# Kernel optimization log

Measured on AMD Instinct MI355X. Metric: run time of the kernel, lower is better.

## Reference

```python
import jax, jax.numpy as jnp
import numpy as np


def setup_inputs() -> dict:
    key = jax.random.key(0)
    b, d, s = 16, 1024, 4096
    x = jax.random.normal(key, (b, d, s), dtype=jnp.float32)
    return {"x": x, "k": 8}


def reference(x, k):
    # k-max pooling over the last axis, preserving original relative order.
    # torch: topk -> argsort(ind) -> gather. Equivalent: take top-k values,
    # then reorder them by ascending original index.
    vals, idx = jax.lax.top_k(x, k)            # [b, d, k]
    order = jnp.argsort(idx, axis=-1)          # positions that sort original indices ascending
    out = jnp.take_along_axis(vals, order, axis=-1)  # [b, d, k] in original order
    return out
```

## Files before the change

### kernel.cpp

```cpp
#include <hip/hip_runtime.h>
#include <stdint.h>

#define WPB    4
#define CAP    256
#define KK     8
#define SLEN   4096
#define CHUNKS 16

__global__ __launch_bounds__(256, 3)
void kmax_kernel(const float* __restrict__ x, float* __restrict__ out, int nrows) {
    const int wave = threadIdx.x >> 6;
    const int lane = threadIdx.x & 63;
    const int row  = blockIdx.x * WPB + wave;
    const bool active = row < nrows;

    __shared__ int s_cnt[WPB];
    __shared__ unsigned long long s_key[WPB][CAP];

    if (lane == 0) s_cnt[wave] = 0;
    __syncthreads();

    const float NEG_INF = __int_as_float(0xff800000);
    float Tthr = 0.0f;

    if (active) {
        const float4* xr = reinterpret_cast<const float4*>(x + (size_t)row * SLEN);
        float4 f[CHUNKS];
        #pragma unroll
        for (int j = 0; j < CHUNKS; ++j)
            f[j] = xr[j * 64 + lane];

        float m[8];
        #pragma unroll
        for (int e = 0; e < 8; ++e) m[e] = NEG_INF;
        #pragma unroll
        for (int j = 0; j < CHUNKS; ++j) {
            const int b = (j & 1) * 4;
            m[b + 0] = fmaxf(m[b + 0], f[j].x);
            m[b + 1] = fmaxf(m[b + 1], f[j].y);
            m[b + 2] = fmaxf(m[b + 2], f[j].z);
            m[b + 3] = fmaxf(m[b + 3], f[j].w);
        }

        #define MCAS(a, b) { float hi = fmaxf(m[a], m[b]); float lo = fminf(m[a], m[b]); m[a] = hi; m[b] = lo; }
        MCAS(0,1) MCAS(2,3) MCAS(4,5) MCAS(6,7)
        MCAS(0,2) MCAS(1,3) MCAS(4,6) MCAS(5,7)
        MCAS(1,2) MCAS(5,6)
        MCAS(0,4) MCAS(1,5) MCAS(2,6) MCAS(3,7)
        MCAS(2,4) MCAS(3,5)
        MCAS(1,2) MCAS(3,4) MCAS(5,6)
        #undef MCAS

        #pragma unroll
        for (int s = 1; s < 64; s <<= 1) {
            float b[8], t[8];
            #pragma unroll
            for (int i = 0; i < 8; ++i) b[i] = __shfl_xor(m[i], s, 64);
            #pragma unroll
            for (int i = 0; i < 8; ++i) t[i] = fmaxf(m[i], b[7 - i]);
            #define BCAS(a, c) { float hi = fmaxf(t[a], t[c]); float lo = fminf(t[a], t[c]); t[a] = hi; t[c] = lo; }
            BCAS(0,4) BCAS(1,5) BCAS(2,6) BCAS(3,7)
            BCAS(0,2) BCAS(1,3) BCAS(4,6) BCAS(5,7)
            BCAS(0,1) BCAS(2,3) BCAS(4,5) BCAS(6,7)
            #undef BCAS
            #pragma unroll
            for (int i = 0; i < 8; ++i) m[i] = t[i];
        }
        Tthr = m[7];

        #pragma unroll
        for (int j = 0; j < CHUNKS; ++j) {
            const float4 v = f[j];
            const bool p0 = v.x >= Tthr, p1 = v.y >= Tthr, p2 = v.z >= Tthr, p3 = v.w >= Tthr;
            if (p0 || p1 || p2 || p3) {
                const int base = (j * 64 + lane) * 4;
                #define PUSH(val, idx) { \
                    int p = atomicAdd(&s_cnt[wave], 1); \
                    if (p < CAP) { \
                        unsigned u = __float_as_uint(val); \
                        u ^= ((unsigned)((int)u >> 31)) | 0x80000000u; \
                        s_key[wave][p] = ((unsigned long long)u << 32) | (unsigned)(4095 - (idx)); \
                    } }
                if (p0) PUSH(v.x, base + 0)
                if (p1) PUSH(v.y, base + 1)
                if (p2) PUSH(v.z, base + 2)
                if (p3) PUSH(v.w, base + 3)
                #undef PUSH
            }
        }
    }

    __syncthreads();

    if (active) {
        int n = s_cnt[wave];
        if (n > CAP) n = CAP;

        unsigned long long kk[KK];
        #pragma unroll
        for (int i = 0; i < KK; ++i) kk[i] = 0ull;
        for (int i = 0; i < n; ++i) {
            unsigned long long c = s_key[wave][i];
            if (c > kk[7]) {
                #pragma unroll
                for (int t = 7; t > 0; --t)
                    kk[t] = (c > kk[t - 1]) ? kk[t - 1] : ((c > kk[t]) ? c : kk[t]);
                kk[0] = (c > kk[0]) ? c : kk[0];
            }
        }

        #define ICAS(a, b) { bool sw = (unsigned)kk[a] < (unsigned)kk[b]; \
            unsigned long long hi = sw ? kk[b] : kk[a]; \
            unsigned long long lo = sw ? kk[a] : kk[b]; \
            kk[a] = hi; kk[b] = lo; }
        ICAS(0,1) ICAS(2,3) ICAS(4,5) ICAS(6,7)
        ICAS(0,2) ICAS(1,3) ICAS(4,6) ICAS(5,7)
        ICAS(1,2) ICAS(5,6)
        ICAS(0,4) ICAS(1,5) ICAS(2,6) ICAS(3,7)
        ICAS(2,4) ICAS(3,5)
        ICAS(1,2) ICAS(3,4) ICAS(5,6)
        #undef ICAS

        if (lane == 0) {
            float vals[KK];
            #pragma unroll
            for (int i = 0; i < KK; ++i) {
                unsigned g = (unsigned)(kk[i] >> 32);
                unsigned msk = ((int)g < 0) ? 0x80000000u : 0xFFFFFFFFu;
                vals[i] = __uint_as_float(g ^ msk);
            }
            float4* o = reinterpret_cast<float4*>(out + (size_t)row * KK);
            o[0] = make_float4(vals[0], vals[1], vals[2], vals[3]);
            o[1] = make_float4(vals[4], vals[5], vals[6], vals[7]);
        }
    }
}

extern "C" void kernel_launch(void* const* d_in, const int* in_sizes, int n_in,
                              void* d_out, int out_size, void* d_ws, size_t ws_size,
                              hipStream_t stream) {
    const float* x = (const float*)d_in[0];
    float* out = (float*)d_out;
    const int nrows = out_size / KK;
    const int blocks = (nrows + WPB - 1) / WPB;
    kmax_kernel<<<blocks, 256, 0, stream>>>(x, out, nrows);
}
```

Baseline: 360.1 us.

## Stage rows into LDS via direct global-to-LDS loads, drop block barriers

Each row is now loaded with global_load_lds straight into a per-wave LDS buffer instead of being held in registers. The max-reduction starts after half the loads arrive, and the filtering pass re-reads values from LDS. The block-wide __syncthreads calls are replaced by per-wave waitcnt, and the candidate cap is halved. The goal is lower register pressure and earlier overlap of compute with loads. In exchange, each block now uses about 68KB of LDS, which limits occupancy to about 2 blocks per CU, and launch bounds drop to 2.

Measured after the change: 355.8 us. About the same (-1.2%).

```diff
diff --git a/kernel.cpp b/kernel.cpp
--- a/kernel.cpp
+++ b/kernel.cpp
@@ -2,137 +2,153 @@
 #include <stdint.h>
 
 #define WPB    4
-#define CAP    256
+#define CAP    128
 #define KK     8
 #define SLEN   4096
 #define CHUNKS 16
 
-__global__ __launch_bounds__(256, 3)
+typedef const __attribute__((address_space(1))) uint32_t g_u32;
+typedef __attribute__((address_space(3))) uint32_t l_u32;
+
+__global__ __launch_bounds__(256, 2)
 void kmax_kernel(const float* __restrict__ x, float* __restrict__ out, int nrows) {
     const int wave = threadIdx.x >> 6;
     const int lane = threadIdx.x & 63;
     const int row  = blockIdx.x * WPB + wave;
-    const bool active = row < nrows;
 
-    __shared__ int s_cnt[WPB];
+    __shared__ float              s_row[WPB][SLEN];
+    __shared__ int                s_cnt[WPB];
     __shared__ unsigned long long s_key[WPB][CAP];
 
+    if (row >= nrows) return;
+
     if (lane == 0) s_cnt[wave] = 0;
-    __syncthreads();
+
+    const float* gbase = x + (size_t)row * SLEN;
+    float*       lbase = &s_row[wave][0];
+    #pragma unroll
+    for (int j = 0; j < CHUNKS; ++j) {
+        __builtin_amdgcn_global_load_lds((g_u32*)(gbase + j * 256 + lane * 4),
+                                         (l_u32*)(lbase + j * 256),
+                                         16, 0, 0);
+    }
 
     const float NEG_INF = __int_as_float(0xff800000);
-    float Tthr = 0.0f;
+    float m[8];
+    #pragma unroll
+    for (int e = 0; e < 8; ++e) m[e] = NEG_INF;
 
-    if (active) {
-        const float4* xr = reinterpret_cast<const float4*>(x + (size_t)row * SLEN);
-        float4 f[CHUNKS];
+    const float4* lrow = reinterpret_cast<const float4*>(lbase);
+
+    asm volatile("s_waitcnt vmcnt(8)" ::: "memory");
+    #pragma unroll
+    for (int j = 0; j < 8; ++j) {
+        const float4 v = lrow[j * 64 + lane];
+        const int b = (j & 1) * 4;
+        m[b + 0] = fmaxf(m[b + 0], v.x);
+        m[b + 1] = fmaxf(m[b + 1], v.y);
+        m[b + 2] = fmaxf(m[b + 2], v.z);
+        m[b + 3] = fmaxf(m[b + 3], v.w);
+    }
+    asm volatile("s_waitcnt vmcnt(0)" ::: "memory");
+    #pragma unroll
+    for (int j = 8; j < CHUNKS; ++j) {
+        const float4 v = lrow[j * 64 + lane];
+        const int b = (j & 1) * 4;
+        m[b + 0] = fmaxf(m[b + 0], v.x);
+        m[b + 1] = fmaxf(m[b + 1], v.y);
+        m[b + 2] = fmaxf(m[b + 2], v.z);
+        m[b + 3] = fmaxf(m[b + 3], v.w);
+    }
+
+    #define MCAS(a, b) { float hi = fmaxf(m[a], m[b]); float lo = fminf(m[a], m[b]); m[a] = hi; m[b] = lo; }
+    MCAS(0,1) MCAS(2,3) MCAS(4,5) MCAS(6,7)
+    MCAS(0,2) MCAS(1,3) MCAS(4,6) MCAS(5,7)
+    MCAS(1,2) MCAS(5,6)
+    MCAS(0,4) MCAS(1,5) MCAS(2,6) MCAS(3,7)
+    MCAS(2,4) MCAS(3,5)
+    MCAS(1,2) MCAS(3,4) MCAS(5,6)
+    #undef MCAS
+
+    #pragma unroll
+    for (int s = 1; s < 64; s <<= 1) {
+        float b[8], t[8];
         #pragma unroll
-        for (int j = 0; j < CHUNKS; ++j)
-            f[j] = xr[j * 64 + lane];
+        for (int i = 0; i < 8; ++i) b[i] = __shfl_xor(m[i], s, 64);
+        #pragma unroll
+        for (int i = 0; i < 8; ++i) t[i] = fmaxf(m[i], b[7 - i]);
+        #define BCAS(a, c) { float hi = fmaxf(t[a], t[c]); float lo = fminf(t[a], t[c]); t[a] = hi; t[c] = lo; }
+        BCAS(0,4) BCAS(1,5) BCAS(2,6) BCAS(3,7)
+        BCAS(0,2) BCAS(1,3) BCAS(4,6) BCAS(5,7)
+        BCAS(0,1) BCAS(2,3) BCAS(4,5) BCAS(6,7)
+        #undef BCAS
+        #pragma unroll
+        for (int i = 0; i < 8; ++i) m[i] = t[i];
+    }
+    const float Tthr = m[7];
 
-        float m[8];
-        #pragma unroll
-        for (int e = 0; e < 8; ++e) m[e] = NEG_INF;
-        #pragma unroll
-        for (int j = 0; j < CHUNKS; ++j) {
-            const int b = (j & 1) * 4;
-            m[b + 0] = fmaxf(m[b + 0], f[j].x);
-            m[b + 1] = fmaxf(m[b + 1], f[j].y);
-            m[b + 2] = fmaxf(m[b + 2], f[j].z);
-            m[b + 3] = fmaxf(m[b + 3], f[j].w);
-        }
-
-        #define MCAS(a, b) { float hi = fmaxf(m[a], m[b]); float lo = fminf(m[a], m[b]); m[a] = hi; m[b] = lo; }
-        MCAS(0,1) MCAS(2,3) MCAS(4,5) MCAS(6,7)
-        MCAS(0,2) MCAS(1,3) MCAS(4,6) MCAS(5,7)
-        MCAS(1,2) MCAS(5,6)
-        MCAS(0,4) MCAS(1,5) MCAS(2,6) MCAS(3,7)
-        MCAS(2,4) MCAS(3,5)
-        MCAS(1,2) MCAS(3,4) MCAS(5,6)
-        #undef MCAS
-
-        #pragma unroll
-        for (int s = 1; s < 64; s <<= 1) {
-            float b[8], t[8];
-            #pragma unroll
-            for (int i = 0; i < 8; ++i) b[i] = __shfl_xor(m[i], s, 64);
-            #pragma unroll
-            for (int i = 0; i < 8; ++i) t[i] = fmaxf(m[i], b[7 - i]);
-            #define BCAS(a, c) { float hi = fmaxf(t[a], t[c]); float lo = fminf(t[a], t[c]); t[a] = hi; t[c] = lo; }
-            BCAS(0,4) BCAS(1,5) BCAS(2,6) BCAS(3,7)
-            BCAS(0,2) BCAS(1,3) BCAS(4,6) BCAS(5,7)
-            BCAS(0,1) BCAS(2,3) BCAS(4,5) BCAS(6,7)
-            #undef BCAS
-            #pragma unroll
-            for (int i = 0; i < 8; ++i) m[i] = t[i];
-        }
-        Tthr = m[7];
-
-        #pragma unroll
-        for (int j = 0; j < CHUNKS; ++j) {
-            const float4 v = f[j];
-            const bool p0 = v.x >= Tthr, p1 = v.y >= Tthr, p2 = v.z >= Tthr, p3 = v.w >= Tthr;
-            if (p0 || p1 || p2 || p3) {
-                const int base = (j * 64 + lane) * 4;
-                #define PUSH(val, idx) { \
-                    int p = atomicAdd(&s_cnt[wave], 1); \
-                    if (p < CAP) { \
-                        unsigned u = __float_as_uint(val); \
-                        u ^= ((unsigned)((int)u >> 31)) | 0x80000000u; \
-                        s_key[wave][p] = ((unsigned long long)u << 32) | (unsigned)(4095 - (idx)); \
-                    } }
-                if (p0) PUSH(v.x, base + 0)
-                if (p1) PUSH(v.y, base + 1)
-                if (p2) PUSH(v.z, base + 2)
-                if (p3) PUSH(v.w, base + 3)
-                #undef PUSH
-            }
+    #pragma unroll
+    for (int j = 0; j < CHUNKS; ++j) {
+        const float4 v = lrow[j * 64 + lane];
+        const bool p0 = v.x >= Tthr, p1 = v.y >= Tthr, p2 = v.z >= Tthr, p3 = v.w >= Tthr;
+        if (p0 || p1 || p2 || p3) {
+            const int base = (j * 64 + lane) * 4;
+            #define PUSH(val, idx) { \
+                int p = atomicAdd(&s_cnt[wave], 1); \
+                if (p < CAP) { \
+                    unsigned u = __float_as_uint(val); \
+                    u ^= ((unsigned)((int)u >> 31)) | 0x80000000u; \
+                    s_key[wave][p] = ((unsigned long long)u << 32) | (unsigned)(4095 - (idx)); \
+                } }
+            if (p0) PUSH(v.x, base + 0)
+            if (p1) PUSH(v.y, base + 1)
+            if (p2) PUSH(v.z, base + 2)
+            if (p3) PUSH(v.w, base + 3)
+            #undef PUSH
         }
     }
 
-    __syncthreads();
+    asm volatile("s_waitcnt lgkmcnt(0)" ::: "memory");
 
-    if (active) {
-        int n = s_cnt[wave];
-        if (n > CAP) n = CAP;
+    int n = s_cnt[wave];
+    if (n > CAP) n = CAP;
 
-        unsigned long long kk[KK];
+    unsigned long long kk[KK];
+    #pragma unroll
+    for (int i = 0; i < KK; ++i) kk[i] = 0ull;
+    for (int i = 0; i < n; ++i) {
+        unsigned long long c = s_key[wave][i];
+        if (c > kk[7]) {
+            #pragma unroll
+            for (int t = 7; t > 0; --t)
+                kk[t] = (c > kk[t - 1]) ? kk[t - 1] : ((c > kk[t]) ? c : kk[t]);
+            kk[0] = (c > kk[0]) ? c : kk[0];
+        }
+    }
+
+    #define ICAS(a, b) { bool sw = (unsigned)kk[a] < (unsigned)kk[b]; \
+        unsigned long long hi = sw ? kk[b] : kk[a]; \
+        unsigned long long lo = sw ? kk[a] : kk[b]; \
+        kk[a] = hi; kk[b] = lo; }
+    ICAS(0,1) ICAS(2,3) ICAS(4,5) ICAS(6,7)
+    ICAS(0,2) ICAS(1,3) ICAS(4,6) ICAS(5,7)
+    ICAS(1,2) ICAS(5,6)
+    ICAS(0,4) ICAS(1,5) ICAS(2,6) ICAS(3,7)
+    ICAS(2,4) ICAS(3,5)
+    ICAS(1,2) ICAS(3,4) ICAS(5,6)
+    #undef ICAS
+
+    if (lane == 0) {
+        float vals[KK];
         #pragma unroll
-        for (int i = 0; i < KK; ++i) kk[i] = 0ull;
-        for (int i = 0; i < n; ++i) {
-            unsigned long long c = s_key[wave][i];
-            if (c > kk[7]) {
-                #pragma unroll
-                for (int t = 7; t > 0; --t)
-                    kk[t] = (c > kk[t - 1]) ? kk[t - 1] : ((c > kk[t]) ? c : kk[t]);
-                kk[0] = (c > kk[0]) ? c : kk[0];
-            }
+        for (int i = 0; i < KK; ++i) {
+            unsigned g = (unsigned)(kk[i] >> 32);
+            unsigned msk = ((int)g < 0) ? 0x80000000u : 0xFFFFFFFFu;
+            vals[i] = __uint_as_float(g ^ msk);
         }
-
-        #define ICAS(a, b) { bool sw = (unsigned)kk[a] < (unsigned)kk[b]; \
-            unsigned long long hi = sw ? kk[b] : kk[a]; \
-            unsigned long long lo = sw ? kk[a] : kk[b]; \
-            kk[a] = hi; kk[b] = lo; }
-        ICAS(0,1) ICAS(2,3) ICAS(4,5) ICAS(6,7)
-        ICAS(0,2) ICAS(1,3) ICAS(4,6) ICAS(5,7)
-        ICAS(1,2) ICAS(5,6)
-        ICAS(0,4) ICAS(1,5) ICAS(2,6) ICAS(3,7)
-        ICAS(2,4) ICAS(3,5)
-        ICAS(1,2) ICAS(3,4) ICAS(5,6)
-        #undef ICAS
-
-        if (lane == 0) {
-            float vals[KK];
-            #pragma unroll
-            for (int i = 0; i < KK; ++i) {
-                unsigned g = (unsigned)(kk[i] >> 32);
-                unsigned msk = ((int)g < 0) ? 0x80000000u : 0xFFFFFFFFu;
-                vals[i] = __uint_as_float(g ^ msk);
-            }
-            float4* o = reinterpret_cast<float4*>(out + (size_t)row * KK);
-            o[0] = make_float4(vals[0], vals[1], vals[2], vals[3]);
-            o[1] = make_float4(vals[4], vals[5], vals[6], vals[7]);
-        }
+        float4* o = reinterpret_cast<float4*>(out + (size_t)row * KK);
+        o[0] = make_float4(vals[0], vals[1], vals[2], vals[3]);
+        o[1] = make_float4(vals[4], vals[5], vals[6], vals[7]);
     }
 }
 
```

## Estimate threshold from first quarter of row and stream remaining chunks

Applied to the files above, without the earlier changes.

The top-8 threshold is now computed from only the first 1024 elements of each row, not the whole row. The remaining 3072 elements are streamed in 256-float4 chunks and filtered against that threshold, so each lane holds 16 floats instead of 64. This lowers register pressure and lets launch bounds request double the occupancy. Block-wide __syncthreads are replaced by early exit plus a per-wave LDS wait. The looser threshold lets more candidates through, so the candidate buffer (reduced to 192) could overflow on adversarial data.

Result: slower. 369.7 us (+2.7%).

```diff
diff --git a/kernel.cpp b/kernel.cpp
--- a/kernel.cpp
+++ b/kernel.cpp
@@ -1,138 +1,136 @@
 #include <hip/hip_runtime.h>
 #include <stdint.h>
 
-#define WPB    4
-#define CAP    256
-#define KK     8
-#define SLEN   4096
-#define CHUNKS 16
+#define WPB  4
+#define CAP  192
+#define KK   8
+#define SLEN 4096
 
-__global__ __launch_bounds__(256, 3)
+__global__ __launch_bounds__(256, 6)
 void kmax_kernel(const float* __restrict__ x, float* __restrict__ out, int nrows) {
     const int wave = threadIdx.x >> 6;
     const int lane = threadIdx.x & 63;
     const int row  = blockIdx.x * WPB + wave;
-    const bool active = row < nrows;
 
-    __shared__ int s_cnt[WPB];
+    __shared__ int                s_cnt[WPB];
     __shared__ unsigned long long s_key[WPB][CAP];
 
+    if (row >= nrows) return;
     if (lane == 0) s_cnt[wave] = 0;
-    __syncthreads();
 
-    const float NEG_INF = __int_as_float(0xff800000);
-    float Tthr = 0.0f;
+    const float4* xr = reinterpret_cast<const float4*>(x + (size_t)row * SLEN);
 
-    if (active) {
-        const float4* xr = reinterpret_cast<const float4*>(x + (size_t)row * SLEN);
-        float4 f[CHUNKS];
+    float4 c0[4];
+    #pragma unroll
+    for (int j = 0; j < 4; ++j) c0[j] = xr[j * 64 + lane];
+
+    float m[8];
+    m[0] = fmaxf(c0[0].x, c0[2].x);  m[1] = fmaxf(c0[0].y, c0[2].y);
+    m[2] = fmaxf(c0[0].z, c0[2].z);  m[3] = fmaxf(c0[0].w, c0[2].w);
+    m[4] = fmaxf(c0[1].x, c0[3].x);  m[5] = fmaxf(c0[1].y, c0[3].y);
+    m[6] = fmaxf(c0[1].z, c0[3].z);  m[7] = fmaxf(c0[1].w, c0[3].w);
+
+    #define MCAS(a, b) { float hi = fmaxf(m[a], m[b]); float lo = fminf(m[a], m[b]); m[a] = hi; m[b] = lo; }
+    MCAS(0,1) MCAS(2,3) MCAS(4,5) MCAS(6,7)
+    MCAS(0,2) MCAS(1,3) MCAS(4,6) MCAS(5,7)
+    MCAS(1,2) MCAS(5,6)
+    MCAS(0,4) MCAS(1,5) MCAS(2,6) MCAS(3,7)
+    MCAS(2,4) MCAS(3,5)
+    MCAS(1,2) MCAS(3,4) MCAS(5,6)
+    #undef MCAS
+
+    #pragma unroll
+    for (int s = 1; s < 64; s <<= 1) {
+        float b[8], t[8];
         #pragma unroll
-        for (int j = 0; j < CHUNKS; ++j)
-            f[j] = xr[j * 64 + lane];
+        for (int i = 0; i < 8; ++i) b[i] = __shfl_xor(m[i], s, 64);
+        #pragma unroll
+        for (int i = 0; i < 8; ++i) t[i] = fmaxf(m[i], b[7 - i]);
+        #define BCAS(a, c) { float hi = fmaxf(t[a], t[c]); float lo = fminf(t[a], t[c]); t[a] = hi; t[c] = lo; }
+        BCAS(0,4) BCAS(1,5) BCAS(2,6) BCAS(3,7)
+        BCAS(0,2) BCAS(1,3) BCAS(4,6) BCAS(5,7)
+        BCAS(0,1) BCAS(2,3) BCAS(4,5) BCAS(6,7)
+        #undef BCAS
+        #pragma unroll
+        for (int i = 0; i < 8; ++i) m[i] = t[i];
+    }
+    const float T1 = m[7];
 
-        float m[8];
+    #define PUSH(val, idx) { \
+        int p = atomicAdd(&s_cnt[wave], 1); \
+        if (p < CAP) { \
+            unsigned u = __float_as_uint(val); \
+            u ^= ((unsigned)((int)u >> 31)) | 0x80000000u; \
+            s_key[wave][p] = ((unsigned long long)u << 32) | (unsigned)(4095 - (idx)); \
+        } }
+
+    #pragma unroll
+    for (int j = 0; j < 4; ++j) {
+        const float4 v = c0[j];
+        const int base = (j * 64 + lane) * 4;
+        if (v.x >= T1) PUSH(v.x, base + 0)
+        if (v.y >= T1) PUSH(v.y, base + 1)
+        if (v.z >= T1) PUSH(v.z, base + 2)
+        if (v.w >= T1) PUSH(v.w, base + 3)
+    }
+
+    #pragma unroll
+    for (int c = 1; c < 4; ++c) {
+        float4 v[4];
         #pragma unroll
-        for (int e = 0; e < 8; ++e) m[e] = NEG_INF;
+        for (int j = 0; j < 4; ++j) v[j] = xr[c * 256 + j * 64 + lane];
         #pragma unroll
-        for (int j = 0; j < CHUNKS; ++j) {
-            const int b = (j & 1) * 4;
-            m[b + 0] = fmaxf(m[b + 0], f[j].x);
-            m[b + 1] = fmaxf(m[b + 1], f[j].y);
-            m[b + 2] = fmaxf(m[b + 2], f[j].z);
-            m[b + 3] = fmaxf(m[b + 3], f[j].w);
+        for (int j = 0; j < 4; ++j) {
+            const int base = (c * 256 + j * 64 + lane) * 4;
+            if (v[j].x >= T1) PUSH(v[j].x, base + 0)
+            if (v[j].y >= T1) PUSH(v[j].y, base + 1)
+            if (v[j].z >= T1) PUSH(v[j].z, base + 2)
+            if (v[j].w >= T1) PUSH(v[j].w, base + 3)
         }
+    }
+    #undef PUSH
 
-        #define MCAS(a, b) { float hi = fmaxf(m[a], m[b]); float lo = fminf(m[a], m[b]); m[a] = hi; m[b] = lo; }
-        MCAS(0,1) MCAS(2,3) MCAS(4,5) MCAS(6,7)
-        MCAS(0,2) MCAS(1,3) MCAS(4,6) MCAS(5,7)
-        MCAS(1,2) MCAS(5,6)
-        MCAS(0,4) MCAS(1,5) MCAS(2,6) MCAS(3,7)
-        MCAS(2,4) MCAS(3,5)
-        MCAS(1,2) MCAS(3,4) MCAS(5,6)
-        #undef MCAS
+    asm volatile("s_waitcnt lgkmcnt(0)" ::: "memory");
 
-        #pragma unroll
-        for (int s = 1; s < 64; s <<= 1) {
-            float b[8], t[8];
+    int n = s_cnt[wave];
+    if (n > CAP) n = CAP;
+
+    unsigned long long kk[KK];
+    #pragma unroll
+    for (int i = 0; i < KK; ++i) kk[i] = 0ull;
+    for (int i = 0; i < n; ++i) {
+        unsigned long long c = s_key[wave][i];
+        if (c > kk[7]) {
             #pragma unroll
-            for (int i = 0; i < 8; ++i) b[i] = __shfl_xor(m[i], s, 64);
-            #pragma unroll
-            for (int i = 0; i < 8; ++i) t[i] = fmaxf(m[i], b[7 - i]);
-            #define BCAS(a, c) { float hi = fmaxf(t[a], t[c]); float lo = fminf(t[a], t[c]); t[a] = hi; t[c] = lo; }
-            BCAS(0,4) BCAS(1,5) BCAS(2,6) BCAS(3,7)
-            BCAS(0,2) BCAS(1,3) BCAS(4,6) BCAS(5,7)
-            BCAS(0,1) BCAS(2,3) BCAS(4,5) BCAS(6,7)
-            #undef BCAS
-            #pragma unroll
-            for (int i = 0; i < 8; ++i) m[i] = t[i];
-        }
-        Tthr = m[7];
-
-        #pragma unroll
-        for (int j = 0; j < CHUNKS; ++j) {
-            const float4 v = f[j];
-            const bool p0 = v.x >= Tthr, p1 = v.y >= Tthr, p2 = v.z >= Tthr, p3 = v.w >= Tthr;
-            if (p0 || p1 || p2 || p3) {
-                const int base = (j * 64 + lane) * 4;
-                #define PUSH(val, idx) { \
-                    int p = atomicAdd(&s_cnt[wave], 1); \
-                    if (p < CAP) { \
-                        unsigned u = __float_as_uint(val); \
-                        u ^= ((unsigned)((int)u >> 31)) | 0x80000000u; \
-                        s_key[wave][p] = ((unsigned long long)u << 32) | (unsigned)(4095 - (idx)); \
-                    } }
-                if (p0) PUSH(v.x, base + 0)
-                if (p1) PUSH(v.y, base + 1)
-                if (p2) PUSH(v.z, base + 2)
-                if (p3) PUSH(v.w, base + 3)
-                #undef PUSH
-            }
+            for (int t = 7; t > 0; --t)
+                kk[t] = (c > kk[t - 1]) ? kk[t - 1] : ((c > kk[t]) ? c : kk[t]);
+            kk[0] = (c > kk[0]) ? c : kk[0];
         }
     }
 
-    __syncthreads();
+    #define ICAS(a, b) { bool sw = (unsigned)kk[a] < (unsigned)kk[b]; \
+        unsigned long long hi = sw ? kk[b] : kk[a]; \
+        unsigned long long lo = sw ? kk[a] : kk[b]; \
+        kk[a] = hi; kk[b] = lo; }
+    ICAS(0,1) ICAS(2,3) ICAS(4,5) ICAS(6,7)
+    ICAS(0,2) ICAS(1,3) ICAS(4,6) ICAS(5,7)
+    ICAS(1,2) ICAS(5,6)
+    ICAS(0,4) ICAS(1,5) ICAS(2,6) ICAS(3,7)
+    ICAS(2,4) ICAS(3,5)
+    ICAS(1,2) ICAS(3,4) ICAS(5,6)
+    #undef ICAS
 
-    if (active) {
-        int n = s_cnt[wave];
-        if (n > CAP) n = CAP;
-
-        unsigned long long kk[KK];
+    if (lane == 0) {
+        float vals[KK];
         #pragma unroll
-        for (int i = 0; i < KK; ++i) kk[i] = 0ull;
-        for (int i = 0; i < n; ++i) {
-            unsigned long long c = s_key[wave][i];
-            if (c > kk[7]) {
-                #pragma unroll
-                for (int t = 7; t > 0; --t)
-                    kk[t] = (c > kk[t - 1]) ? kk[t - 1] : ((c > kk[t]) ? c : kk[t]);
-                kk[0] = (c > kk[0]) ? c : kk[0];
-            }
+        for (int i = 0; i < KK; ++i) {
+            unsigned g = (unsigned)(kk[i] >> 32);
+            unsigned msk = ((int)g < 0) ? 0x80000000u : 0xFFFFFFFFu;
+            vals[i] = __uint_as_float(g ^ msk);
         }
-
-        #define ICAS(a, b) { bool sw = (unsigned)kk[a] < (unsigned)kk[b]; \
-            unsigned long long hi = sw ? kk[b] : kk[a]; \
-            unsigned long long lo = sw ? kk[a] : kk[b]; \
-            kk[a] = hi; kk[b] = lo; }
-        ICAS(0,1) ICAS(2,3) ICAS(4,5) ICAS(6,7)
-        ICAS(0,2) ICAS(1,3) ICAS(4,6) ICAS(5,7)
-        ICAS(1,2) ICAS(5,6)
-        ICAS(0,4) ICAS(1,5) ICAS(2,6) ICAS(3,7)
-        ICAS(2,4) ICAS(3,5)
-        ICAS(1,2) ICAS(3,4) ICAS(5,6)
-        #undef ICAS
-
-        if (lane == 0) {
-            float vals[KK];
-            #pragma unroll
-            for (int i = 0; i < KK; ++i) {
-                unsigned g = (unsigned)(kk[i] >> 32);
-                unsigned msk = ((int)g < 0) ? 0x80000000u : 0xFFFFFFFFu;
-                vals[i] = __uint_as_float(g ^ msk);
-            }
-            float4* o = reinterpret_cast<float4*>(out + (size_t)row * KK);
-            o[0] = make_float4(vals[0], vals[1], vals[2], vals[3]);
-            o[1] = make_float4(vals[4], vals[5], vals[6], vals[7]);
-        }
+        float4* o = reinterpret_cast<float4*>(out + (size_t)row * KK);
+        o[0] = make_float4(vals[0], vals[1], vals[2], vals[3]);
+        o[1] = make_float4(vals[4], vals[5], vals[6], vals[7]);
     }
 }
 
```
